# Kernel tuning notes

Hardware: AMD Instinct MI355X
Metric: run time of the kernel (lower is better)

## Reference

```python
import jax, jax.numpy as jnp
import numpy as np

NEG_SLOPE = 0.2
BN_EPS = 1e-5


def _gatv2(x, src, dst, Wl, Wr, att, b, N, concat):
    # x: [N, Cin]; src/dst: [E] (self-loops already appended)
    H, F = att.shape
    xl = (x @ Wl).reshape(N, H, F)  # source transform
    xr = (x @ Wr).reshape(N, H, F)  # target transform
    s = jax.nn.leaky_relu(xl[src] + xr[dst], NEG_SLOPE)  # [E,H,F]
    e = jnp.einsum('ehf,hf->eh', s, att)                  # [E,H]
    m = jax.ops.segment_max(e, dst, num_segments=N)       # [N,H]
    ex = jnp.exp(e - m[dst])
    den = jax.ops.segment_sum(ex, dst, num_segments=N)
    alpha = ex / den[dst]                                 # [E,H] softmax over in-edges
    out = jax.ops.segment_sum(alpha[:, :, None] * xl[src], dst, num_segments=N)  # [N,H,F]
    out = out.reshape(N, H * F) if concat else out.mean(axis=1)
    return out + b


def _bn_eval(x, g, b, rm, rv):
    return (x - rm) * jax.lax.rsqrt(rv + BN_EPS) * g + b


def setup_inputs() -> dict:
    key = jax.random.key(0)
    ks = jax.random.split(key, 16)
    N, E, Cin, Fh, H, Cout = 50000, 800000, 128, 64, 4, 128
    Hm = H * Fh  # 256
    d = {
        'x': jax.random.normal(ks[0], (N, Cin), jnp.float32),
        'edge_index': jax.random.randint(ks[1], (2, E), 0, N, jnp.int64),
        'Wl1': jax.random.normal(ks[2], (Cin, Hm), jnp.float32) / np.sqrt(Cin),
        'Wr1': jax.random.normal(ks[3], (Cin, Hm), jnp.float32) / np.sqrt(Cin),
        'att1': jax.random.normal(ks[4], (H, Fh), jnp.float32) / np.sqrt(Fh),
        'b1': jnp.zeros((Hm,), jnp.float32),
        'bn1_g': jax.random.uniform(ks[5], (Hm,), jnp.float32, 0.5, 1.5),
        'bn1_b': 0.1 * jax.random.normal(ks[6], (Hm,), jnp.float32),
        'bn1_m': jnp.zeros((Hm,), jnp.float32),
        'bn1_v': jnp.ones((Hm,), jnp.float32),
        'Wl2': jax.random.normal(ks[7], (Hm, Hm), jnp.float32) / np.sqrt(Hm),
        'Wr2': jax.random.normal(ks[8], (Hm, Hm), jnp.float32) / np.sqrt(Hm),
        'att2': jax.random.normal(ks[9], (H, Fh), jnp.float32) / np.sqrt(Fh),
        'b2': jnp.zeros((Hm,), jnp.float32),
        'bn2_g': jax.random.uniform(ks[10], (Hm,), jnp.float32, 0.5, 1.5),
        'bn2_b': 0.1 * jax.random.normal(ks[11], (Hm,), jnp.float32),
        'bn2_m': jnp.zeros((Hm,), jnp.float32),
        'bn2_v': jnp.ones((Hm,), jnp.float32),
        'Wl3': jax.random.normal(ks[12], (Hm, Cout), jnp.float32) / np.sqrt(Hm),
        'Wr3': jax.random.normal(ks[13], (Hm, Cout), jnp.float32) / np.sqrt(Hm),
        'att3': jax.random.normal(ks[14], (1, Cout), jnp.float32) / np.sqrt(Cout),
        'b3': jnp.zeros((Cout,), jnp.float32),
    }
    return d


def reference(x, edge_index, Wl1, Wr1, att1, b1, bn1_g, bn1_b, bn1_m, bn1_v,
              Wl2, Wr2, att2, b2, bn2_g, bn2_b, bn2_m, bn2_v,
              Wl3, Wr3, att3, b3):
    N = x.shape[0]
    loop = jnp.arange(N, dtype=edge_index.dtype)
    src = jnp.concatenate([edge_index[0], loop])  # add self-loops (PyG default)
    dst = jnp.concatenate([edge_index[1], loop])
    h = _gatv2(x, src, dst, Wl1, Wr1, att1, b1, N, True)
    h = jax.nn.elu(_bn_eval(h, bn1_g, bn1_b, bn1_m, bn1_v))  # dropout=identity (eval)
    h = _gatv2(h, src, dst, Wl2, Wr2, att2, b2, N, True)
    h = jax.nn.elu(_bn_eval(h, bn2_g, bn2_b, bn2_m, bn2_v))
    return _gatv2(h, src, dst, Wl3, Wr3, att3, b3, N, False)
```

## Files before the change

kernel.cpp:

```cpp
#include <hip/hip_runtime.h>
#include <math.h>

#define NEG_SLOPE 0.2f
#define BN_EPS 1e-5f
#define LOG2E 1.44269504f

typedef _Float16 f16x8 __attribute__((ext_vector_type(8)));
typedef float f32x4 __attribute__((ext_vector_type(4)));
typedef _Float16 h2 __attribute__((ext_vector_type(2)));

union F8 { f16x8 v; h2 h[4]; _Float16 s[8]; uint4 u; };

__device__ __forceinline__ void async_copy16(const void* g, void* l) {
  __builtin_amdgcn_global_load_lds(
      (const __attribute__((address_space(1))) void*)g,
      (__attribute__((address_space(3))) void*)l, 16, 0, 0);
}

__device__ __forceinline__ unsigned int pack2f(float a, float b) {
  union { unsigned int u; _Float16 h[2]; } c;
  c.h[0] = (_Float16)a; c.h[1] = (_Float16)b; return c.u;
}

__device__ __forceinline__ float fdot2f(h2 a, h2 b, float c) {
#if __has_builtin(__builtin_amdgcn_fdot2)
  return __builtin_amdgcn_fdot2(a, b, c, false);
#else
  return fmaf((float)a[0], (float)b[0], fmaf((float)a[1], (float)b[1], c));
#endif
}

template <int CTRL>
__device__ __forceinline__ float dpp_xadd(float x) {
  int yi = __builtin_amdgcn_mov_dpp(__builtin_bit_cast(int, x), CTRL, 0xF, 0xF, true);
  return x + __builtin_bit_cast(float, yi);
}

__global__ void k_f2h(const float* __restrict__ in, unsigned int* __restrict__ out, int n2) {
  int i = blockIdx.x * blockDim.x + threadIdx.x;
  if (i < n2) {
    float2 v = reinterpret_cast<const float2*>(in)[i];
    out[i] = pack2f(v.x, v.y);
  }
}

__global__ __launch_bounds__(256) void k_prep_w3(
    const float* __restrict__ Wl1, const float* __restrict__ Wr1,
    const float* __restrict__ Wl2, const float* __restrict__ Wr2,
    const float* __restrict__ Wl3, const float* __restrict__ Wr3,
    int Cin, int Hm, int Cout,
    _Float16* __restrict__ WT1, _Float16* __restrict__ WT2, _Float16* __restrict__ WT3) {
  int i = blockIdx.x * 256 + threadIdx.x;
  int n1 = 2 * Hm * Cin, n2 = 2 * Hm * Hm, n3 = 2 * Cout * Hm;
  if (i < n1) {
    int c = i / Cin, k = i % Cin;
    float v = (c < Hm) ? Wl1[(size_t)k * Hm + c] : Wr1[(size_t)k * Hm + (c - Hm)];
    WT1[i] = (_Float16)v;
    return;
  }
  i -= n1;
  if (i < n2) {
    int c = i / Hm, k = i % Hm;
    float v = (c < Hm) ? Wl2[(size_t)k * Hm + c] : Wr2[(size_t)k * Hm + (c - Hm)];
    WT2[i] = (_Float16)v;
    return;
  }
  i -= n2;
  if (i < n3) {
    int c = i / Hm, k = i % Hm;
    float v = (c < Cout) ? Wl3[(size_t)k * Cout + c] : Wr3[(size_t)k * Cout + (c - Cout)];
    WT3[i] = (_Float16)v;
  }
}

__global__ __launch_bounds__(256) void k_prep_misc(
    const float* __restrict__ att1, const float* __restrict__ att2, const float* __restrict__ att3,
    const float* __restrict__ b1, const float* __restrict__ g1, const float* __restrict__ bb1,
    const float* __restrict__ m1, const float* __restrict__ v1,
    const float* __restrict__ b2, const float* __restrict__ g2, const float* __restrict__ bb2,
    const float* __restrict__ m2, const float* __restrict__ v2,
    _Float16* __restrict__ a16_1, _Float16* __restrict__ a16_2, _Float16* __restrict__ a16_3,
    float* __restrict__ sc1, float* __restrict__ sh1,
    float* __restrict__ sc2, float* __restrict__ sh2) {
  int c = threadIdx.x;
  a16_1[c] = (_Float16)(att1[c] * LOG2E);
  a16_2[c] = (_Float16)(att2[c] * LOG2E);
  if (c < 128) a16_3[c] = (_Float16)(att3[c] * LOG2E);
  float s = g1[c] * rsqrtf(v1[c] + BN_EPS);
  sc1[c] = s; sh1[c] = (b1[c] - m1[c]) * s + bb1[c];
  s = g2[c] * rsqrtf(v2[c] + BN_EPS);
  sc2[c] = s; sh2[c] = (b2[c] - m2[c]) * s + bb2[c];
}

__global__ void k_count(const int* __restrict__ ei, int E, int N, int* __restrict__ deg) {
  int e = blockIdx.x * blockDim.x + threadIdx.x;
  int T = E + N;
  if (e >= T) return;
  int d = (e < E) ? ei[E + e] : (e - E);
  atomicAdd(&deg[d], 1);
}

__global__ __launch_bounds__(256) void k_bsum(const int* __restrict__ deg, int N,
                                              int* __restrict__ bsum) {
  int t = threadIdx.x;
  int i = blockIdx.x * 256 + t;
  int v = (i < N) ? deg[i] : 0;
  #pragma unroll
  for (int off = 32; off > 0; off >>= 1) v += __shfl_xor(v, off, 64);
  __shared__ int ws[4];
  if ((t & 63) == 0) ws[t >> 6] = v;
  __syncthreads();
  if (t == 0) bsum[blockIdx.x] = ws[0] + ws[1] + ws[2] + ws[3];
}

__global__ __launch_bounds__(1024) void k_bscan(int* __restrict__ bsum, int nb, int N,
                                                int* __restrict__ offs) {
  int t = threadIdx.x;
  int lane = t & 63, w = t >> 6;
  int v = (t < nb) ? bsum[t] : 0;
  int val = v;
  #pragma unroll
  for (int off = 1; off < 64; off <<= 1) {
    int x = __shfl_up(val, off, 64);
    if (lane >= off) val += x;
  }
  __shared__ int ws[16];
  if (lane == 63) ws[w] = val;
  __syncthreads();
  if (w == 0) {
    int s = (lane < 16) ? ws[lane] : 0;
    #pragma unroll
    for (int off = 1; off < 16; off <<= 1) {
      int x = __shfl_up(s, off, 64);
      if (lane >= off) s += x;
    }
    if (lane < 16) ws[lane] = s;
  }
  __syncthreads();
  int excl = (w > 0 ? ws[w - 1] : 0) + val - v;
  if (t < nb) bsum[t] = excl;
  if (t == nb - 1) offs[N] = excl + v;
}

__global__ __launch_bounds__(256) void k_boffs(const int* __restrict__ deg, int N,
                                               const int* __restrict__ bpre,
                                               int* __restrict__ offs, int* __restrict__ cursor) {
  int t = threadIdx.x;
  int i = blockIdx.x * 256 + t;
  int lane = t & 63, w = t >> 6;
  int v = (i < N) ? deg[i] : 0;
  int val = v;
  #pragma unroll
  for (int off = 1; off < 64; off <<= 1) {
    int x = __shfl_up(val, off, 64);
    if (lane >= off) val += x;
  }
  __shared__ int ws[4];
  if (lane == 63) ws[w] = val;
  __syncthreads();
  int wo = 0;
  #pragma unroll
  for (int k = 0; k < 4; ++k) if (k < w) wo += ws[k];
  int excl = bpre[blockIdx.x] + wo + val - v;
  if (i < N) { offs[i] = excl; cursor[i] = excl; }
}

__global__ void k_scatter(const int* __restrict__ ei, int E, int N,
                          int* __restrict__ cursor, int* __restrict__ csr_src) {
  int e = blockIdx.x * blockDim.x + threadIdx.x;
  int T = E + N;
  if (e < 32) csr_src[T + e] = 0;
  if (e >= T) return;
  int s, d;
  if (e < E) { s = ei[e]; d = ei[E + e]; } else { s = d = e - E; }
  int pos = atomicAdd(&cursor[d], 1);
  csr_src[pos] = s;
}

__global__ __launch_bounds__(512) void k_hgemm(const _Float16* __restrict__ A,
                                               const _Float16* __restrict__ BT,
                                               _Float16* __restrict__ C,
                                               int M, int Ntot, int K) {
  __shared__ _Float16 As[2][128 * 64];
  __shared__ _Float16 Bs[2][256 * 64];
  const int t = threadIdx.x;
  const int lane = t & 63, w = t >> 6;
  const int wr = w >> 2, wc = w & 3;
  const int bm0 = blockIdx.x * 128, bn0 = blockIdx.y * 256;
  f32x4 acc[4][4] = {};
  const int nkt = K >> 6;

  auto stage = [&](int b, int kt) {
    #pragma unroll
    for (int i = 0; i < 2; ++i) {
      int q = i * 512 + t;
      int row = q >> 3, sl = q & 7;
      int ssrc = sl ^ (row & 7);
      int ga = bm0 + row; if (ga >= M) ga = M - 1;
      async_copy16(&A[(size_t)ga * K + kt * 64 + ssrc * 8], &As[b][q * 8]);
    }
    #pragma unroll
    for (int i = 0; i < 4; ++i) {
      int q = i * 512 + t;
      int row = q >> 3, sl = q & 7;
      int ssrc = sl ^ (row & 7);
      async_copy16(&BT[(size_t)(bn0 + row) * K + kt * 64 + ssrc * 8], &Bs[b][q * 8]);
    }
  };

  stage(0, 0);
  for (int kt = 0; kt < nkt; ++kt) {
    int cur = kt & 1;
    if (kt + 1 < nkt) {
      stage(cur ^ 1, kt + 1);
      asm volatile("s_waitcnt vmcnt(6)" ::: "memory");
    } else {
      asm volatile("s_waitcnt vmcnt(0)" ::: "memory");
    }
    __builtin_amdgcn_s_barrier();
    #pragma unroll
    for (int ks = 0; ks < 2; ++ks) {
      f16x8 a[4], b[4];
      const int sl = ks * 4 + (lane >> 4);
      #pragma unroll
      for (int mi = 0; mi < 4; ++mi) {
        int row = wr * 64 + mi * 16 + (lane & 15);
        a[mi] = *(const f16x8*)&As[cur][(row * 8 + (sl ^ (row & 7))) * 8];
      }
      #pragma unroll
      for (int ni = 0; ni < 4; ++ni) {
        int row = wc * 64 + ni * 16 + (lane & 15);
        b[ni] = *(const f16x8*)&Bs[cur][(row * 8 + (sl ^ (row & 7))) * 8];
      }
      #pragma unroll
      for (int mi = 0; mi < 4; ++mi)
        #pragma unroll
        for (int ni = 0; ni < 4; ++ni)
          acc[mi][ni] = __builtin_amdgcn_mfma_f32_16x16x32_f16(a[mi], b[ni], acc[mi][ni], 0, 0, 0);
    }
    __builtin_amdgcn_s_barrier();
  }
  const int r0 = (lane >> 4) * 4;
  const int cc = lane & 15;
  #pragma unroll
  for (int mi = 0; mi < 4; ++mi) {
    #pragma unroll
    for (int r = 0; r < 4; ++r) {
      int row = bm0 + wr * 64 + mi * 16 + r0 + r;
      if (row >= M) continue;
      #pragma unroll
      for (int ni = 0; ni < 4; ++ni) {
        int col = bn0 + wc * 64 + ni * 16 + cc;
        C[(size_t)row * Ntot + col] = (_Float16)acc[mi][ni][r];
      }
    }
  }
}

__global__ __launch_bounds__(64) void k_gat4(
    const _Float16* __restrict__ xlr,
    const _Float16* __restrict__ att16,
    const float* __restrict__ sc, const float* __restrict__ sh,
    const int* __restrict__ offs, const int* __restrict__ csr,
    _Float16* __restrict__ hout) {
  const int n = blockIdx.x;
  const int lane = threadIdx.x;
  const int sub = lane & 15;
  const int qi = lane >> 4;
  const unsigned subB = (unsigned)sub << 5;
  const char* __restrict__ xc = (const char*)xlr;

  F8 at0, at1, xr0, xr1;
  at0.u = *(const uint4*)((const char*)att16 + subB);
  at1.u = *(const uint4*)((const char*)att16 + subB + 16);
  {
    unsigned xro = (unsigned)n * 1024u + 512u + subB;
    xr0.u = *(const uint4*)(xc + xro);
    xr1.u = *(const uint4*)(xc + xro + 16);
  }
  const h2 k02 = {(_Float16)NEG_SLOPE, (_Float16)NEG_SLOPE};
  const int j0 = offs[n], j1 = offs[n + 1];

  float m = -INFINITY, l = 0.f;
  float acc[16];
  #pragma unroll
  for (int i = 0; i < 16; ++i) acc[i] = 0.f;

  unsigned o0 = (unsigned)csr[j0 + qi] * 1024u + subB;
  unsigned o1 = (unsigned)csr[j0 + 4 + qi] * 1024u + subB;
  unsigned o2 = (unsigned)csr[j0 + 8 + qi] * 1024u + subB;
  F8 v0, v1, n0, n1;
  v0.u = *(const uint4*)(xc + o0);
  v1.u = *(const uint4*)(xc + o0 + 16);
  n0.u = *(const uint4*)(xc + o1);
  n1.u = *(const uint4*)(xc + o1 + 16);

  for (int j = j0; j < j1; j += 4) {
    F8 f0, f1;
    f0.u = *(const uint4*)(xc + o2);
    f1.u = *(const uint4*)(xc + o2 + 16);
    int c3 = csr[j + 12 + qi];

    float e = 0.f;
    #pragma unroll
    for (int r = 0; r < 4; ++r) {
      h2 s0 = v0.h[r] + xr0.h[r];
      s0 = __builtin_elementwise_max(s0, s0 * k02);
      e = fdot2f(s0, at0.h[r], e);
      h2 s1 = v1.h[r] + xr1.h[r];
      s1 = __builtin_elementwise_max(s1, s1 * k02);
      e = fdot2f(s1, at1.h[r], e);
    }
    e = dpp_xadd<0xB1>(e);
    e = dpp_xadd<0x4E>(e);
    if (j + qi >= j1) e = -1e30f;

    if (__any(e > m + 11.5f)) {
      float mc = fmaxf(m, e);
      mc = fmaxf(mc, __shfl_xor(mc, 16, 64));
      mc = fmaxf(mc, __shfl_xor(mc, 32, 64));
      float c0 = exp2f(m - mc);
      l *= c0;
      #pragma unroll
      for (int i = 0; i < 16; ++i) acc[i] *= c0;
      m = mc;
    }
    float p = exp2f(e - m);
    l += p;
    #pragma unroll
    for (int i = 0; i < 8; ++i) acc[i] = fmaf(p, (float)v0.s[i], acc[i]);
    #pragma unroll
    for (int i = 0; i < 8; ++i) acc[8 + i] = fmaf(p, (float)v1.s[i], acc[8 + i]);
    v0 = n0; v1 = n1; n0 = f0; n1 = f1;
    o2 = (unsigned)c3 * 1024u + subB;
  }
  l += __shfl_xor(l, 16, 64);
  l += __shfl_xor(l, 32, 64);
  #pragma unroll
  for (int i = 0; i < 16; ++i) {
    acc[i] += __shfl_xor(acc[i], 16, 64);
    acc[i] += __shfl_xor(acc[i], 32, 64);
  }
  if (qi == 0) {
    float inv = 1.f / l;
    const float4* sc4 = (const float4*)sc;
    const float4* sh4 = (const float4*)sh;
    float ov[16];
    #pragma unroll
    for (int k = 0; k < 4; ++k) {
      float4 s4 = sc4[4 * sub + k], t4 = sh4[4 * sub + k];
      ov[4 * k + 0] = acc[4 * k + 0] * inv * s4.x + t4.x;
      ov[4 * k + 1] = acc[4 * k + 1] * inv * s4.y + t4.y;
      ov[4 * k + 2] = acc[4 * k + 2] * inv * s4.z + t4.z;
      ov[4 * k + 3] = acc[4 * k + 3] * inv * s4.w + t4.w;
    }
    #pragma unroll
    for (int i = 0; i < 16; ++i) ov[i] = ov[i] > 0.f ? ov[i] : (__expf(ov[i]) - 1.f);
    F8 o0h, o1h;
    #pragma unroll
    for (int i = 0; i < 8; ++i) { o0h.s[i] = (_Float16)ov[i]; o1h.s[i] = (_Float16)ov[8 + i]; }
    F8* ob = (F8*)hout;
    ob[(size_t)n * 32 + 2 * sub] = o0h;
    ob[(size_t)n * 32 + 2 * sub + 1] = o1h;
  }
}

__global__ __launch_bounds__(64) void k_gat1(
    const _Float16* __restrict__ xlr,
    const _Float16* __restrict__ att16,
    const float* __restrict__ bias,
    const int* __restrict__ offs, const int* __restrict__ csr,
    float* __restrict__ out) {
  const int n = blockIdx.x;
  const int lane = threadIdx.x;
  const int sub = lane & 7;
  const int gi = lane >> 3;
  const unsigned subB = (unsigned)sub << 5;
  const char* __restrict__ xc = (const char*)xlr;

  F8 at0, at1, xr0, xr1;
  at0.u = *(const uint4*)((const char*)att16 + subB);
  at1.u = *(const uint4*)((const char*)att16 + subB + 16);
  {
    unsigned xro = (unsigned)n * 512u + 256u + subB;
    xr0.u = *(const uint4*)(xc + xro);
    xr1.u = *(const uint4*)(xc + xro + 16);
  }
  const h2 k02 = {(_Float16)NEG_SLOPE, (_Float16)NEG_SLOPE};
  const int j0 = offs[n], j1 = offs[n + 1];

  float m = -INFINITY, l = 0.f;
  float acc[16];
  #pragma unroll
  for (int i = 0; i < 16; ++i) acc[i] = 0.f;

  unsigned o0 = (unsigned)csr[j0 + gi] * 512u + subB;
  unsigned o1 = (unsigned)csr[j0 + 8 + gi] * 512u + subB;
  unsigned o2 = (unsigned)csr[j0 + 16 + gi] * 512u + subB;
  F8 v0, v1, n0, n1;
  v0.u = *(const uint4*)(xc + o0);
  v1.u = *(const uint4*)(xc + o0 + 16);
  n0.u = *(const uint4*)(xc + o1);
  n1.u = *(const uint4*)(xc + o1 + 16);

  for (int j = j0; j < j1; j += 8) {
    F8 f0, f1;
    f0.u = *(const uint4*)(xc + o2);
    f1.u = *(const uint4*)(xc + o2 + 16);
    int c3 = csr[j + 24 + gi];

    float e = 0.f;
    #pragma unroll
    for (int r = 0; r < 4; ++r) {
      h2 s0 = v0.h[r] + xr0.h[r];
      s0 = __builtin_elementwise_max(s0, s0 * k02);
      e = fdot2f(s0, at0.h[r], e);
      h2 s1 = v1.h[r] + xr1.h[r];
      s1 = __builtin_elementwise_max(s1, s1 * k02);
      e = fdot2f(s1, at1.h[r], e);
    }
    e = dpp_xadd<0xB1>(e);
    e = dpp_xadd<0x4E>(e);
    e += __shfl_xor(e, 4, 64);
    if (j + gi >= j1) e = -1e30f;

    if (__any(e > m + 11.5f)) {
      float mc = fmaxf(m, e);
      mc = fmaxf(mc, __shfl_xor(mc, 8, 64));
      mc = fmaxf(mc, __shfl_xor(mc, 16, 64));
      mc = fmaxf(mc, __shfl_xor(mc, 32, 64));
      float c0 = exp2f(m - mc);
      l *= c0;
      #pragma unroll
      for (int i = 0; i < 16; ++i) acc[i] *= c0;
      m = mc;
    }
    float p = exp2f(e - m);
    l += p;
    #pragma unroll
    for (int i = 0; i < 8; ++i) acc[i] = fmaf(p, (float)v0.s[i], acc[i]);
    #pragma unroll
    for (int i = 0; i < 8; ++i) acc[8 + i] = fmaf(p, (float)v1.s[i], acc[8 + i]);
    v0 = n0; v1 = n1; n0 = f0; n1 = f1;
    o2 = (unsigned)c3 * 512u + subB;
  }
  l += __shfl_xor(l, 8, 64);
  l += __shfl_xor(l, 16, 64);
  l += __shfl_xor(l, 32, 64);
  #pragma unroll
  for (int i = 0; i < 16; ++i) {
    acc[i] += __shfl_xor(acc[i], 8, 64);
    acc[i] += __shfl_xor(acc[i], 16, 64);
    acc[i] += __shfl_xor(acc[i], 32, 64);
  }
  if (gi == 0) {
    float inv = 1.f / l;
    const float4* b4 = (const float4*)bias;
    float4* ob = (float4*)out;
    #pragma unroll
    for (int k = 0; k < 4; ++k) {
      float4 bb = b4[4 * sub + k];
      float4 o;
      o.x = acc[4 * k + 0] * inv + bb.x;
      o.y = acc[4 * k + 1] * inv + bb.y;
      o.z = acc[4 * k + 2] * inv + bb.z;
      o.w = acc[4 * k + 3] * inv + bb.w;
      ob[(size_t)n * 32 + 4 * sub + k] = o;
    }
  }
}

extern "C" void kernel_launch(void* const* d_in, const int* in_sizes, int n_in,
                              void* d_out, int out_size, void* d_ws, size_t ws_size,
                              hipStream_t stream) {
  const float* x    = (const float*)d_in[0];
  const int*   ei   = (const int*)d_in[1];
  const float* Wl1  = (const float*)d_in[2];
  const float* Wr1  = (const float*)d_in[3];
  const float* att1 = (const float*)d_in[4];
  const float* b1   = (const float*)d_in[5];
  const float* bn1g = (const float*)d_in[6];
  const float* bn1b = (const float*)d_in[7];
  const float* bn1m = (const float*)d_in[8];
  const float* bn1v = (const float*)d_in[9];
  const float* Wl2  = (const float*)d_in[10];
  const float* Wr2  = (const float*)d_in[11];
  const float* att2 = (const float*)d_in[12];
  const float* b2   = (const float*)d_in[13];
  const float* bn2g = (const float*)d_in[14];
  const float* bn2b = (const float*)d_in[15];
  const float* bn2m = (const float*)d_in[16];
  const float* bn2v = (const float*)d_in[17];
  const float* Wl3  = (const float*)d_in[18];
  const float* Wr3  = (const float*)d_in[19];
  const float* att3 = (const float*)d_in[20];
  const float* b3   = (const float*)d_in[21];

  const int Hm   = in_sizes[5];
  const int Cout = in_sizes[21];
  const int Cin  = in_sizes[2] / Hm;
  const int N    = in_sizes[0] / Cin;
  const int E    = in_sizes[1] / 2;
  const int T    = E + N;

  _Float16* x16 = (_Float16*)d_ws;
  _Float16* h   = x16 + (size_t)N * Cin;
  _Float16* xlr = h + (size_t)N * Hm;
  _Float16* WT1 = xlr + (size_t)N * 2 * Hm;
  _Float16* WT2 = WT1 + (size_t)2 * Hm * Cin;
  _Float16* WT3 = WT2 + (size_t)2 * Hm * Hm;
  _Float16* a16_1 = WT3 + (size_t)2 * Cout * Hm;
  _Float16* a16_2 = a16_1 + 256;
  _Float16* a16_3 = a16_2 + 256;
  float* sc1 = (float*)(a16_3 + 128);
  float* sh1 = sc1 + 256;
  float* sc2 = sh1 + 256;
  float* sh2 = sc2 + 256;
  int* deg    = (int*)(sh2 + 256);
  int* offs   = deg + N;
  int* cursor = offs + N + 1;
  int* csr    = cursor + N;
  int* bsum   = csr + T + 32;

  const int nb = (N + 255) / 256;

  hipMemsetAsync(deg, 0, (size_t)N * sizeof(int), stream);
  k_count<<<(T + 255) / 256, 256, 0, stream>>>(ei, E, N, deg);
  k_bsum<<<nb, 256, 0, stream>>>(deg, N, bsum);
  k_bscan<<<1, 1024, 0, stream>>>(bsum, nb, N, offs);
  k_boffs<<<nb, 256, 0, stream>>>(deg, N, bsum, offs, cursor);
  k_scatter<<<(T + 255) / 256, 256, 0, stream>>>(ei, E, N, cursor, csr);

  int n2 = N * Cin / 2;
  k_f2h<<<(n2 + 255) / 256, 256, 0, stream>>>(x, (unsigned int*)x16, n2);
  int wtot = 2 * Hm * Cin + 2 * Hm * Hm + 2 * Cout * Hm;
  k_prep_w3<<<(wtot + 255) / 256, 256, 0, stream>>>(Wl1, Wr1, Wl2, Wr2, Wl3, Wr3,
                                                    Cin, Hm, Cout, WT1, WT2, WT3);
  k_prep_misc<<<1, 256, 0, stream>>>(att1, att2, att3,
                                     b1, bn1g, bn1b, bn1m, bn1v,
                                     b2, bn2g, bn2b, bn2m, bn2v,
                                     a16_1, a16_2, a16_3, sc1, sh1, sc2, sh2);

  const int mb = (N + 127) / 128;

  k_hgemm<<<dim3(mb, 2 * Hm / 256), 512, 0, stream>>>(x16, WT1, xlr, N, 2 * Hm, Cin);
  k_gat4<<<N, 64, 0, stream>>>(xlr, a16_1, sc1, sh1, offs, csr, h);

  k_hgemm<<<dim3(mb, 2 * Hm / 256), 512, 0, stream>>>(h, WT2, xlr, N, 2 * Hm, Hm);
  k_gat4<<<N, 64, 0, stream>>>(xlr, a16_2, sc2, sh2, offs, csr, h);

  k_hgemm<<<dim3(mb, 2 * Cout / 256), 512, 0, stream>>>(h, WT3, xlr, N, 2 * Cout, Hm);
  k_gat1<<<N, 64, 0, stream>>>(xlr, a16_3, b3, offs, csr, (float*)d_out);
}
```

Measured before the change: 425.9 us.

## Fold self-loops into GAT kernels, merge prep kernels, pack 4 nodes per block

Self-loop edges are no longer added to the CSR. Each GAT kernel instead seeds its online softmax state (max, sum, accumulator) from the node's own self-edge score and features. The three prep kernels (x conversion, weight transpose, misc params) are merged into one launch. The GAT kernels now run 4 nodes per 256-thread block instead of one 64-thread block per node, which cuts launch and scheduling overhead. The risk is that degree counting and scatter now skip self-loops, so correctness depends on the seeded initialization matching the old softmax exactly.

```diff
diff --git a/kernel.cpp b/kernel.cpp
--- a/kernel.cpp
+++ b/kernel.cpp
@@ -36,44 +36,13 @@
   return x + __builtin_bit_cast(float, yi);
 }
 
-__global__ void k_f2h(const float* __restrict__ in, unsigned int* __restrict__ out, int n2) {
-  int i = blockIdx.x * blockDim.x + threadIdx.x;
-  if (i < n2) {
-    float2 v = reinterpret_cast<const float2*>(in)[i];
-    out[i] = pack2f(v.x, v.y);
-  }
-}
-
-__global__ __launch_bounds__(256) void k_prep_w3(
+__global__ __launch_bounds__(256) void k_prep_all(
+    const float* __restrict__ x, unsigned int* __restrict__ x16u, int n2,
     const float* __restrict__ Wl1, const float* __restrict__ Wr1,
     const float* __restrict__ Wl2, const float* __restrict__ Wr2,
     const float* __restrict__ Wl3, const float* __restrict__ Wr3,
     int Cin, int Hm, int Cout,
-    _Float16* __restrict__ WT1, _Float16* __restrict__ WT2, _Float16* __restrict__ WT3) {
-  int i = blockIdx.x * 256 + threadIdx.x;
-  int n1 = 2 * Hm * Cin, n2 = 2 * Hm * Hm, n3 = 2 * Cout * Hm;
-  if (i < n1) {
-    int c = i / Cin, k = i % Cin;
-    float v = (c < Hm) ? Wl1[(size_t)k * Hm + c] : Wr1[(size_t)k * Hm + (c - Hm)];
-    WT1[i] = (_Float16)v;
-    return;
-  }
-  i -= n1;
-  if (i < n2) {
-    int c = i / Hm, k = i % Hm;
-    float v = (c < Hm) ? Wl2[(size_t)k * Hm + c] : Wr2[(size_t)k * Hm + (c - Hm)];
-    WT2[i] = (_Float16)v;
-    return;
-  }
-  i -= n2;
-  if (i < n3) {
-    int c = i / Hm, k = i % Hm;
-    float v = (c < Cout) ? Wl3[(size_t)k * Cout + c] : Wr3[(size_t)k * Cout + (c - Cout)];
-    WT3[i] = (_Float16)v;
-  }
-}
-
-__global__ __launch_bounds__(256) void k_prep_misc(
+    _Float16* __restrict__ WT1, _Float16* __restrict__ WT2, _Float16* __restrict__ WT3,
     const float* __restrict__ att1, const float* __restrict__ att2, const float* __restrict__ att3,
     const float* __restrict__ b1, const float* __restrict__ g1, const float* __restrict__ bb1,
     const float* __restrict__ m1, const float* __restrict__ v1,
@@ -82,22 +51,51 @@
     _Float16* __restrict__ a16_1, _Float16* __restrict__ a16_2, _Float16* __restrict__ a16_3,
     float* __restrict__ sc1, float* __restrict__ sh1,
     float* __restrict__ sc2, float* __restrict__ sh2) {
-  int c = threadIdx.x;
-  a16_1[c] = (_Float16)(att1[c] * LOG2E);
-  a16_2[c] = (_Float16)(att2[c] * LOG2E);
-  if (c < 128) a16_3[c] = (_Float16)(att3[c] * LOG2E);
-  float s = g1[c] * rsqrtf(v1[c] + BN_EPS);
-  sc1[c] = s; sh1[c] = (b1[c] - m1[c]) * s + bb1[c];
-  s = g2[c] * rsqrtf(v2[c] + BN_EPS);
-  sc2[c] = s; sh2[c] = (b2[c] - m2[c]) * s + bb2[c];
-}
-
-__global__ void k_count(const int* __restrict__ ei, int E, int N, int* __restrict__ deg) {
+  int i = blockIdx.x * 256 + threadIdx.x;
+  if (i < n2) {
+    float2 v = reinterpret_cast<const float2*>(x)[i];
+    x16u[i] = pack2f(v.x, v.y);
+    return;
+  }
+  i -= n2;
+  int w1 = 2 * Hm * Cin, w2 = 2 * Hm * Hm, w3 = 2 * Cout * Hm;
+  if (i < w1) {
+    int c = i / Cin, k = i % Cin;
+    float v = (c < Hm) ? Wl1[(size_t)k * Hm + c] : Wr1[(size_t)k * Hm + (c - Hm)];
+    WT1[i] = (_Float16)v;
+    return;
+  }
+  i -= w1;
+  if (i < w2) {
+    int c = i / Hm, k = i % Hm;
+    float v = (c < Hm) ? Wl2[(size_t)k * Hm + c] : Wr2[(size_t)k * Hm + (c - Hm)];
+    WT2[i] = (_Float16)v;
+    return;
+  }
+  i -= w2;
+  if (i < w3) {
+    int c = i / Hm, k = i % Hm;
+    float v = (c < Cout) ? Wl3[(size_t)k * Cout + c] : Wr3[(size_t)k * Cout + (c - Cout)];
+    WT3[i] = (_Float16)v;
+    return;
+  }
+  i -= w3;
+  if (i < 256) {
+    int c = i;
+    a16_1[c] = (_Float16)(att1[c] * LOG2E);
+    a16_2[c] = (_Float16)(att2[c] * LOG2E);
+    if (c < 128) a16_3[c] = (_Float16)(att3[c] * LOG2E);
+    float s = g1[c] * rsqrtf(v1[c] + BN_EPS);
+    sc1[c] = s; sh1[c] = (b1[c] - m1[c]) * s + bb1[c];
+    s = g2[c] * rsqrtf(v2[c] + BN_EPS);
+    sc2[c] = s; sh2[c] = (b2[c] - m2[c]) * s + bb2[c];
+  }
+}
+
+__global__ void k_count(const int* __restrict__ ei, int E, int* __restrict__ deg) {
   int e = blockIdx.x * blockDim.x + threadIdx.x;
-  int T = E + N;
-  if (e >= T) return;
-  int d = (e < E) ? ei[E + e] : (e - E);
-  atomicAdd(&deg[d], 1);
+  if (e >= E) return;
+  atomicAdd(&deg[ei[E + e]], 1);
 }
 
 __global__ __launch_bounds__(256) void k_bsum(const int* __restrict__ deg, int N,
@@ -165,14 +163,12 @@
   if (i < N) { offs[i] = excl; cursor[i] = excl; }
 }
 
-__global__ void k_scatter(const int* __restrict__ ei, int E, int N,
+__global__ void k_scatter(const int* __restrict__ ei, int E,
                           int* __restrict__ cursor, int* __restrict__ csr_src) {
   int e = blockIdx.x * blockDim.x + threadIdx.x;
-  int T = E + N;
-  if (e < 32) csr_src[T + e] = 0;
-  if (e >= T) return;
-  int s, d;
-  if (e < E) { s = ei[e]; d = ei[E + e]; } else { s = d = e - E; }
+  if (e < 32) csr_src[E + e] = 0;
+  if (e >= E) return;
+  int s = ei[e], d = ei[E + e];
   int pos = atomicAdd(&cursor[d], 1);
   csr_src[pos] = s;
 }
@@ -257,14 +253,15 @@
   }
 }
 
-__global__ __launch_bounds__(64) void k_gat4(
+__global__ __launch_bounds__(256) void k_gat4(
     const _Float16* __restrict__ xlr,
     const _Float16* __restrict__ att16,
     const float* __restrict__ sc, const float* __restrict__ sh,
     const int* __restrict__ offs, const int* __restrict__ csr,
-    _Float16* __restrict__ hout) {
-  const int n = blockIdx.x;
-  const int lane = threadIdx.x;
+    int N, _Float16* __restrict__ hout) {
+  const int n = blockIdx.x * 4 + (threadIdx.x >> 6);
+  if (n >= N) return;
+  const int lane = threadIdx.x & 63;
   const int sub = lane & 15;
   const int qi = lane >> 4;
   const unsigned subB = (unsigned)sub << 5;
@@ -281,10 +278,34 @@
   const h2 k02 = {(_Float16)NEG_SLOPE, (_Float16)NEG_SLOPE};
   const int j0 = offs[n], j1 = offs[n + 1];
 
-  float m = -INFINITY, l = 0.f;
+  float m, l;
   float acc[16];
-  #pragma unroll
-  for (int i = 0; i < 16; ++i) acc[i] = 0.f;
+  {
+    F8 sl0, sl1;
+    unsigned xlo = (unsigned)n * 1024u + subB;
+    sl0.u = *(const uint4*)(xc + xlo);
+    sl1.u = *(const uint4*)(xc + xlo + 16);
+    float es = 0.f;
+    #pragma unroll
+    for (int r = 0; r < 4; ++r) {
+      h2 s0 = sl0.h[r] + xr0.h[r];
+      s0 = __builtin_elementwise_max(s0, s0 * k02);
+      es = fdot2f(s0, at0.h[r], es);
+      h2 s1 = sl1.h[r] + xr1.h[r];
+      s1 = __builtin_elementwise_max(s1, s1 * k02);
+      es = fdot2f(s1, at1.h[r], es);
+    }
+    es = dpp_xadd<0xB1>(es);
+    es = dpp_xadd<0x4E>(es);
+    m = es;
+    bool q0 = (qi == 0);
+    l = q0 ? 1.f : 0.f;
+    #pragma unroll
+    for (int i = 0; i < 8; ++i) {
+      acc[i]     = q0 ? (float)sl0.s[i] : 0.f;
+      acc[8 + i] = q0 ? (float)sl1.s[i] : 0.f;
+    }
+  }
 
   unsigned o0 = (unsigned)csr[j0 + qi] * 1024u + subB;
   unsigned o1 = (unsigned)csr[j0 + 4 + qi] * 1024u + subB;
@@ -365,14 +386,15 @@
   }
 }
 
-__global__ __launch_bounds__(64) void k_gat1(
+__global__ __launch_bounds__(256) void k_gat1(
     const _Float16* __restrict__ xlr,
     const _Float16* __restrict__ att16,
     const float* __restrict__ bias,
     const int* __restrict__ offs, const int* __restrict__ csr,
-    float* __restrict__ out) {
-  const int n = blockIdx.x;
-  const int lane = threadIdx.x;
+    int N, float* __restrict__ out) {
+  const int n = blockIdx.x * 4 + (threadIdx.x >> 6);
+  if (n >= N) return;
+  const int lane = threadIdx.x & 63;
   const int sub = lane & 7;
   const int gi = lane >> 3;
   const unsigned subB = (unsigned)sub << 5;
@@ -389,10 +411,35 @@
   const h2 k02 = {(_Float16)NEG_SLOPE, (_Float16)NEG_SLOPE};
   const int j0 = offs[n], j1 = offs[n + 1];
 
-  float m = -INFINITY, l = 0.f;
+  float m, l;
   float acc[16];
-  #pragma unroll
-  for (int i = 0; i < 16; ++i) acc[i] = 0.f;
+  {
+    F8 sl0, sl1;
+    unsigned xlo = (unsigned)n * 512u + subB;
+    sl0.u = *(const uint4*)(xc + xlo);
+    sl1.u = *(const uint4*)(xc + xlo + 16);
+    float es = 0.f;
+    #pragma unroll
+    for (int r = 0; r < 4; ++r) {
+      h2 s0 = sl0.h[r] + xr0.h[r];
+      s0 = __builtin_elementwise_max(s0, s0 * k02);
+      es = fdot2f(s0, at0.h[r], es);
+      h2 s1 = sl1.h[r] + xr1.h[r];
+      s1 = __builtin_elementwise_max(s1, s1 * k02);
+      es = fdot2f(s1, at1.h[r], es);
+    }
+    es = dpp_xadd<0xB1>(es);
+    es = dpp_xadd<0x4E>(es);
+    es += __shfl_xor(es, 4, 64);
+    m = es;
+    bool g0 = (gi == 0);
+    l = g0 ? 1.f : 0.f;
+    #pragma unroll
+    for (int i = 0; i < 8; ++i) {
+      acc[i]     = g0 ? (float)sl0.s[i] : 0.f;
+      acc[8 + i] = g0 ? (float)sl1.s[i] : 0.f;
+    }
+  }
 
   unsigned o0 = (unsigned)csr[j0 + gi] * 512u + subB;
   unsigned o1 = (unsigned)csr[j0 + 8 + gi] * 512u + subB;
@@ -501,7 +548,6 @@
   const int Cin  = in_sizes[2] / Hm;
   const int N    = in_sizes[0] / Cin;
   const int E    = in_sizes[1] / 2;
-  const int T    = E + N;
 
   _Float16* x16 = (_Float16*)d_ws;
   _Float16* h   = x16 + (size_t)N * Cin;
@@ -520,35 +566,37 @@
   int* offs   = deg + N;
   int* cursor = offs + N + 1;
   int* csr    = cursor + N;
-  int* bsum   = csr + T + 32;
+  int* bsum   = csr + E + 32;
 
   const int nb = (N + 255) / 256;
 
   hipMemsetAsync(deg, 0, (size_t)N * sizeof(int), stream);
-  k_count<<<(T + 255) / 256, 256, 0, stream>>>(ei, E, N, deg);
+  k_count<<<(E + 255) / 256, 256, 0, stream>>>(ei, E, deg);
   k_bsum<<<nb, 256, 0, stream>>>(deg, N, bsum);
   k_bscan<<<1, 1024, 0, stream>>>(bsum, nb, N, offs);
   k_boffs<<<nb, 256, 0, stream>>>(deg, N, bsum, offs, cursor);
-  k_scatter<<<(T + 255) / 256, 256, 0, stream>>>(ei, E, N, cursor, csr);
+  k_scatter<<<(E + 255) / 256, 256, 0, stream>>>(ei, E, cursor, csr);
 
   int n2 = N * Cin / 2;
-  k_f2h<<<(n2 + 255) / 256, 256, 0, stream>>>(x, (unsigned int*)x16, n2);
   int wtot = 2 * Hm * Cin + 2 * Hm * Hm + 2 * Cout * Hm;
-  k_prep_w3<<<(wtot + 255) / 256, 256, 0, stream>>>(Wl1, Wr1, Wl2, Wr2, Wl3, Wr3,
-                                                    Cin, Hm, Cout, WT1, WT2, WT3);
-  k_prep_misc<<<1, 256, 0, stream>>>(att1, att2, att3,
-                                     b1, bn1g, bn1b, bn1m, bn1v,
-                                     b2, bn2g, bn2b, bn2m, bn2v,
-                                     a16_1, a16_2, a16_3, sc1, sh1, sc2, sh2);
+  int ptot = n2 + wtot + 256;
+  k_prep_all<<<(ptot + 255) / 256, 256, 0, stream>>>(
+      x, (unsigned int*)x16, n2,
+      Wl1, Wr1, Wl2, Wr2, Wl3, Wr3, Cin, Hm, Cout, WT1, WT2, WT3,
+      att1, att2, att3,
+      b1, bn1g, bn1b, bn1m, bn1v,
+      b2, bn2g, bn2b, bn2m, bn2v,
+      a16_1, a16_2, a16_3, sc1, sh1, sc2, sh2);
 
   const int mb = (N + 127) / 128;
+  const int gb = (N + 3) / 4;
 
   k_hgemm<<<dim3(mb, 2 * Hm / 256), 512, 0, stream>>>(x16, WT1, xlr, N, 2 * Hm, Cin);
-  k_gat4<<<N, 64, 0, stream>>>(xlr, a16_1, sc1, sh1, offs, csr, h);
+  k_gat4<<<gb, 256, 0, stream>>>(xlr, a16_1, sc1, sh1, offs, csr, N, h);
 
   k_hgemm<<<dim3(mb, 2 * Hm / 256), 512, 0, stream>>>(h, WT2, xlr, N, 2 * Hm, Hm);
-  k_gat4<<<N, 64, 0, stream>>>(xlr, a16_2, sc2, sh2, offs, csr, h);
+  k_gat4<<<gb, 256, 0, stream>>>(xlr, a16_2, sc2, sh2, offs, csr, N, h);
 
   k_hgemm<<<dim3(mb, 2 * Cout / 256), 512, 0, stream>>>(h, WT3, xlr, N, 2 * Cout, Hm);
-  k_gat1<<<N, 64, 0, stream>>>(xlr, a16_3, b3, offs, csr, (float*)d_out);
-}
+  k_gat1<<<gb, 256, 0, stream>>>(xlr, a16_3, b3, offs, csr, N, (float*)d_out);
+}
```

Measured after the change: 389.1 us. -8.7%, faster.
